# Kernel optimization log

Measured on AMD Instinct MI355X. Metric: run time of the kernel, lower is better.

The kernel has to match this reference:

```python
import jax, jax.numpy as jnp
import numpy as np
import itertools

B, N, K, G = 1024, 1024, 6, 720  # G = K!
H1, H2, C = 64, 32, 40
IN = K * 3


def setup_inputs() -> dict:
    key = jax.random.key(0)
    ks = jax.random.split(key, 8)
    x = jax.random.normal(ks[0], (B, N, 3), dtype=jnp.float32)
    # per-sample subsample indices (torch uses randperm(N)[:K]; distinctness
    # is irrelevant to the math, randint keeps them in-range)
    idx = jax.random.randint(ks[1], (B, K), 0, N)
    perms = jnp.asarray(
        np.array(list(itertools.permutations(range(K))), dtype=np.int32)
    )  # (G, K)
    # MLP params: torch Linear default init ~ U(-1/sqrt(fan_in), 1/sqrt(fan_in))
    def lin(k, fin, fout):
        kw, kb = jax.random.split(k)
        s = 1.0 / np.sqrt(fin)
        W = jax.random.uniform(kw, (fin, fout), jnp.float32, -s, s)
        b = jax.random.uniform(kb, (fout,), jnp.float32, -s, s)
        return W, b
    W1, b1 = lin(ks[2], IN, H1)
    W2, b2 = lin(ks[3], H1, H2)
    W3, b3 = lin(ks[4], H2, C)
    return dict(x=x, W1=W1, b1=b1, W2=W2, b2=b2, W3=W3, b3=b3,
                idx=idx, perms=perms)


def reference(x, W1, b1, W2, b2, W3, b3, idx, perms):
    Bv = x.shape[0]
    Gv, Kv = perms.shape
    # gather the K subsampled points per batch element: (B, K, 3)
    pts = jnp.take_along_axis(x, idx[:, :, None], axis=1)
    # expand over all K! permutations of the point ordering: (B, G, K, 3)
    permuted = pts[:, perms, :]
    flat = permuted.reshape(Bv, Gv, Kv * 3)  # (B, G, K*3)
    h = jax.nn.relu(flat @ W1 + b1)          # (B, G, H1)
    h = jax.nn.relu(h @ W2 + b2)             # (B, G, H2)
    y = h @ W3 + b3                          # (B, G, C)
    return y.mean(axis=1)                    # (B, C)
```

## Files before the change

kernel.cpp:

```cpp
#include <hip/hip_runtime.h>
#include <hip/hip_bf16.h>

typedef __attribute__((ext_vector_type(8))) short short8;
typedef __attribute__((ext_vector_type(4))) float f32x4;
typedef unsigned int u32;
typedef __attribute__((ext_vector_type(4))) unsigned int u32x4;

#define NN 1024

#define LFENCE { asm volatile("s_waitcnt lgkmcnt(0)" ::: "memory"); __builtin_amdgcn_sched_barrier(0); }

#define PKROW(DST, TA, TB) { \
  float va_ = fmaxf(bx_ + (TA), 0.0f), vb_ = fmaxf(bx_ + (TB), 0.0f); \
  asm("v_cvt_pk_bf16_f32 %0, %1, %2" : "=v"(DST) : "v"(va_), "v"(vb_)); }

#define PK3(KA,KB,KC, BX) { const float bx_ = (BX); \
  PKROW(KA, T0_, T1_) PKROW(KB, T2_, T3_) PKROW(KC, T4_, T5_) }

#define SGCOMP(A0,A1,A2, M0,M1,M2) { \
  const float f0_ = b1v + P[(A0)*6+0]; \
  const float f1_ = b1v + P[(A1)*6+0]; \
  const float f2_ = b1v + P[(A2)*6+0]; \
  const float g12_ = P[(A1)*6+1] + P[(A2)*6+2]; \
  const float g21_ = P[(A2)*6+1] + P[(A1)*6+2]; \
  const float g02_ = P[(A0)*6+1] + P[(A2)*6+2]; \
  const float g20_ = P[(A2)*6+1] + P[(A0)*6+2]; \
  const float g01_ = P[(A0)*6+1] + P[(A1)*6+2]; \
  const float g10_ = P[(A1)*6+1] + P[(A0)*6+2]; \
  const float e0_ = P[(M0)*6+3], e1_ = P[(M1)*6+3], e2_ = P[(M2)*6+3]; \
  const float h12_ = P[(M1)*6+4] + P[(M2)*6+5]; \
  const float h21_ = P[(M2)*6+4] + P[(M1)*6+5]; \
  const float h02_ = P[(M0)*6+4] + P[(M2)*6+5]; \
  const float h20_ = P[(M2)*6+4] + P[(M0)*6+5]; \
  const float h01_ = P[(M0)*6+4] + P[(M1)*6+5]; \
  const float h10_ = P[(M1)*6+4] + P[(M0)*6+5]; \
  const float T0_ = e0_+h12_, T1_ = e0_+h21_, T2_ = e1_+h02_; \
  const float T3_ = e1_+h20_, T4_ = e2_+h01_, T5_ = e2_+h10_; \
  PK3(k0,k1,k2,   f0_+g12_)  PK3(k3,k4,k5,   f0_+g21_) \
  PK3(k6,k7,k8,   f1_+g02_)  PK3(k9,k10,k11, f1_+g20_) \
  PK3(k12,k13,k14,f2_+g01_)  PK3(k15,k16,k17,f2_+g10_) }

#define WRT16(BB) { \
  bp0[(BB+0)*64]=k0;  bp0[(BB+8)*64]=k8;  \
  bp1[(BB+1)*64]=k1;  bp1[(BB+9)*64]=k9;  \
  bp2[(BB+2)*64]=k2;  bp2[(BB+10)*64]=k10; \
  bp3[(BB+3)*64]=k3;  bp3[(BB+11)*64]=k11; \
  bp4[(BB+4)*64]=k4;  bp4[(BB+12)*64]=k12; \
  bp5[(BB+5)*64]=k5;  bp5[(BB+13)*64]=k13; \
  bp6[(BB+6)*64]=k6;  bp6[(BB+14)*64]=k14; \
  bp7[(BB+7)*64]=k7;  bp7[(BB+15)*64]=k15; }

#define WOV(RA, RB) { \
  wb[(RA)*64 + (lane ^ ((((RA)) & 7) << 3))] = k16; \
  wb[(RB)*64 + (lane ^ ((((RB)) & 7) << 3))] = k17; }

#define MFMA4T(A0_, A1_) do { \
  f32x4 c0_ = {b2v0,b2v0,b2v0,b2v0}; \
  f32x4 c1_ = {b2v1,b2v1,b2v1,b2v1}; \
  c0_ = __builtin_amdgcn_mfma_f32_16x16x32_bf16(A0_, bh00, c0_, 0,0,0); \
  c0_ = __builtin_amdgcn_mfma_f32_16x16x32_bf16(A1_, bh10, c0_, 0,0,0); \
  c1_ = __builtin_amdgcn_mfma_f32_16x16x32_bf16(A0_, bh01, c1_, 0,0,0); \
  c1_ = __builtin_amdgcn_mfma_f32_16x16x32_bf16(A1_, bh11, c1_, 0,0,0); \
  acc0[0]+=fmaxf(c0_[0],0.f); acc0[1]+=fmaxf(c0_[1],0.f); \
  acc0[2]+=fmaxf(c0_[2],0.f); acc0[3]+=fmaxf(c0_[3],0.f); \
  acc1[0]+=fmaxf(c1_[0],0.f); acc1[1]+=fmaxf(c1_[1],0.f); \
  acc1[2]+=fmaxf(c1_[2],0.f); acc1[3]+=fmaxf(c1_[3],0.f); \
} while(0)

#define RQ(B) { \
  q0  = *(const u32x4*)&wb[(B)+e0b];       q1  = *(const u32x4*)&wb[(B)+e0b+4]; \
  q2  = *(const u32x4*)&wb[(B)+e1b];       q3  = *(const u32x4*)&wb[(B)+e1b+4]; \
  q4  = *(const u32x4*)&wb[(B)+512+e0b];   q5  = *(const u32x4*)&wb[(B)+512+e0b+4]; \
  q6  = *(const u32x4*)&wb[(B)+512+e1b];   q7  = *(const u32x4*)&wb[(B)+512+e1b+4]; \
  q8  = *(const u32x4*)&wb[(B)+1024+e0b];  q9  = *(const u32x4*)&wb[(B)+1024+e0b+4]; \
  q10 = *(const u32x4*)&wb[(B)+1024+e1b];  q11 = *(const u32x4*)&wb[(B)+1024+e1b+4]; }

#define FRAG(dst, qa_, qb_) { \
  u32x4 t_; \
  t_[0] = __builtin_amdgcn_perm(qa_[1], qa_[0], sel); \
  t_[1] = __builtin_amdgcn_perm(qa_[3], qa_[2], sel); \
  t_[2] = __builtin_amdgcn_perm(qb_[1], qb_[0], sel); \
  t_[3] = __builtin_amdgcn_perm(qb_[3], qb_[2], sel); \
  dst = __builtin_bit_cast(short8, t_); }

#define M3 { \
  short8 A0f_, A1f_; \
  FRAG(A0f_, q0, q1);   FRAG(A1f_, q2, q3);   MFMA4T(A0f_, A1f_); \
  FRAG(A0f_, q4, q5);   FRAG(A1f_, q6, q7);   MFMA4T(A0f_, A1f_); \
  FRAG(A0f_, q8, q9);   FRAG(A1f_, q10, q11); MFMA4T(A0f_, A1f_); }

#define ZPAD6 { \
  wb[18*64+(lane^16)]=0u; wb[19*64+(lane^24)]=0u; wb[20*64+(lane^32)]=0u; \
  wb[21*64+(lane^40)]=0u; wb[22*64+(lane^48)]=0u; wb[23*64+(lane^56)]=0u; }

#define MKB(dst_h, KH, NIDX) do { \
  _Pragma("unroll") \
  for (int e_ = 0; e_ < 8; ++e_) { \
    float f_ = W2[((KH)*32 + kg*8 + e_)*32 + 16*(NIDX) + colb]; \
    __hip_bfloat16 hi_ = __float2bfloat16(f_); \
    dst_h[e_] = *(short*)&hi_; \
  } \
} while(0)

__global__ __launch_bounds__(256, 2) void symm_mlp_kernel(
    const float* __restrict__ x,
    const float* __restrict__ W1, const float* __restrict__ b1,
    const float* __restrict__ W2, const float* __restrict__ b2,
    const float* __restrict__ W3, const float* __restrict__ b3,
    const int* __restrict__ idx,
    float* __restrict__ out)
{
    __shared__ u32 h1s[4][72 * 64];
    __shared__ float redbuf[4][32];

    const int tid   = threadIdx.x;
    const int lane  = tid & 63;
    const int wv    = tid >> 6;
    const int batch = blockIdx.x;

    int pidx[6];
    #pragma unroll
    for (int k = 0; k < 6; ++k) pidx[k] = idx[batch * 6 + k];

    float px[6][3];
    #pragma unroll
    for (int k = 0; k < 6; ++k)
        #pragma unroll
        for (int d = 0; d < 3; ++d) px[k][d] = x[(batch * NN + pidx[k]) * 3 + d];

    float w1c[18];
    #pragma unroll
    for (int r = 0; r < 18; ++r) w1c[r] = W1[r * 64 + lane];

    const float b1v = b1[lane];
    const int colb = lane & 15, kg = lane >> 4;
    const float b2v0 = b2[colb];
    const float b2v1 = b2[16 + colb];

    short8 bh00, bh10, bh01, bh11;
    MKB(bh00, 0, 0);
    MKB(bh10, 1, 0);
    MKB(bh01, 0, 1);
    MKB(bh11, 1, 1);

    float P[36];
    #pragma unroll
    for (int k = 0; k < 6; ++k)
    #pragma unroll
    for (int j = 0; j < 6; ++j)
        P[k*6+j] = fmaf(px[k][2], w1c[3*j+2], fmaf(px[k][1], w1c[3*j+1], px[k][0] * w1c[3*j+0]));

    u32* wb  = &h1s[wv][0];
    u32* bp0 = wb + (lane ^ 0);
    u32* bp1 = wb + (lane ^ 8);
    u32* bp2 = wb + (lane ^ 16);
    u32* bp3 = wb + (lane ^ 24);
    u32* bp4 = wb + (lane ^ 32);
    u32* bp5 = wb + (lane ^ 40);
    u32* bp6 = wb + (lane ^ 48);
    u32* bp7 = wb + (lane ^ 56);

    const int r2l = (lane & 15) >> 1;
    const int sm  = r2l << 3;
    const int e0b = r2l * 64 + ((kg * 8) ^ sm);
    const int e1b = r2l * 64 + ((32 + kg * 8) ^ sm);
    const u32 sel = (lane & 1) ? 0x07060302u : 0x05040100u;

    f32x4 acc0 = {0.f,0.f,0.f,0.f}, acc1 = {0.f,0.f,0.f,0.f};
    u32x4 q0,q1,q2,q3,q4,q5,q6,q7,q8,q9,q10,q11;
    u32 k0,k1,k2,k3,k4,k5,k6,k7,k8,k9,k10,k11,k12,k13,k14,k15,k16,k17;

    if (wv == 0) {
        SGCOMP(0,1,2, 3,4,5); WRT16(0);  WOV(64,65);
        SGCOMP(0,1,3, 2,4,5); WRT16(16); WOV(66,67);
        SGCOMP(0,1,4, 2,3,5); WRT16(32); WOV(68,69);
        SGCOMP(0,1,5, 2,3,4); WRT16(48); WOV(70,71);
    } else if (wv == 1) {
        SGCOMP(0,2,4, 1,3,5); WRT16(0);  WOV(64,65);
        SGCOMP(0,2,5, 1,3,4); WRT16(16); WOV(66,67);
        SGCOMP(0,3,4, 1,2,5); WRT16(32); WOV(68,69);
        SGCOMP(0,3,5, 1,2,4); WRT16(48); WOV(70,71);
    } else if (wv == 2) {
        SGCOMP(1,2,3, 0,4,5); WRT16(0);  WOV(64,65);
        SGCOMP(1,2,4, 0,3,5); WRT16(16); WOV(66,67);
        SGCOMP(1,2,5, 0,3,4); WRT16(32); WOV(68,69);
        SGCOMP(1,3,4, 0,2,5); WRT16(48); WOV(70,71);
    } else {
        SGCOMP(1,4,5, 0,2,3); WRT16(0);  WOV(64,65);
        SGCOMP(2,3,4, 0,1,5); WRT16(16); WOV(66,67);
        SGCOMP(2,3,5, 0,1,4); WRT16(32); WOV(68,69);
        SGCOMP(2,4,5, 0,1,3); WRT16(48); WOV(70,71);
    }
    RQ(0);    LFENCE; M3;
    RQ(1536);         M3;
    RQ(3072);         M3;

    ZPAD6;
    if (wv == 0)      { SGCOMP(0,2,3, 1,4,5); }
    else if (wv == 1) { SGCOMP(0,4,5, 1,2,3); }
    else if (wv == 2) { SGCOMP(1,3,5, 0,2,4); }
    else              { SGCOMP(3,4,5, 0,1,2); }
    WRT16(0); WOV(16,17);
    RQ(0); LFENCE; M3;

    float s0 = acc0[0] + acc0[1] + acc0[2] + acc0[3];
    float s1 = acc1[0] + acc1[1] + acc1[2] + acc1[3];
    s0 += __shfl_xor(s0, 16, 64);  s0 += __shfl_xor(s0, 32, 64);
    s1 += __shfl_xor(s1, 16, 64);  s1 += __shfl_xor(s1, 32, 64);
    s0 -= 12.0f * fmaxf(b2v0, 0.0f);
    s1 -= 12.0f * fmaxf(b2v1, 0.0f);

    if (lane < 16)       redbuf[wv][lane] = s0;
    else if (lane < 32)  redbuf[wv][lane] = s1;
    __syncthreads();

    if (tid < 40) {
        float m[32];
        #pragma unroll
        for (int c = 0; c < 32; ++c)
            m[c] = (redbuf[0][c] + redbuf[1][c] + redbuf[2][c] + redbuf[3][c]) * (1.0f / 720.0f);
        float y = b3[tid];
        #pragma unroll
        for (int c = 0; c < 32; ++c) y = fmaf(m[c], W3[c * 40 + tid], y);
        out[batch * 40 + tid] = y;
    }
}

extern "C" void kernel_launch(void* const* d_in, const int* in_sizes, int n_in,
                              void* d_out, int out_size, void* d_ws, size_t ws_size,
                              hipStream_t stream) {
    const float* x  = (const float*)d_in[0];
    const float* W1 = (const float*)d_in[1];
    const float* b1 = (const float*)d_in[2];
    const float* W2 = (const float*)d_in[3];
    const float* b2 = (const float*)d_in[4];
    const float* W3 = (const float*)d_in[5];
    const float* b3 = (const float*)d_in[6];
    const int* idx   = (const int*)d_in[7];
    float* out = (float*)d_out;

    symm_mlp_kernel<<<1024, 256, 0, stream>>>(x, W1, b1, W2, b2, W3, b3, idx, out);
}
```

Baseline: 18.98 us.

## Process permutation chunks one at a time in a small LDS buffer

Each wave now builds, stores and consumes one 18-row chunk of first-layer activations at a time, using a 24-row LDS buffer, instead of staging four chunks in a 72-row buffer. The padding rows are zeroed once up front, and the bias-padding correction grows to 60 rows to match. Cutting LDS per block and raising launch bounds to 3 blocks per SM is meant to increase occupancy. In exchange, the per-chunk LDS store, fence and read sequence is serialized five times, so less write/read work can overlap within a wave.

After: 21.68 us. 1.14x slower.

```diff
diff --git a/kernel.cpp b/kernel.cpp
--- a/kernel.cpp
+++ b/kernel.cpp
@@ -40,19 +40,19 @@
   PK3(k6,k7,k8,   f1_+g02_)  PK3(k9,k10,k11, f1_+g20_) \
   PK3(k12,k13,k14,f2_+g01_)  PK3(k15,k16,k17,f2_+g10_) }
 
-#define WRT16(BB) { \
-  bp0[(BB+0)*64]=k0;  bp0[(BB+8)*64]=k8;  \
-  bp1[(BB+1)*64]=k1;  bp1[(BB+9)*64]=k9;  \
-  bp2[(BB+2)*64]=k2;  bp2[(BB+10)*64]=k10; \
-  bp3[(BB+3)*64]=k3;  bp3[(BB+11)*64]=k11; \
-  bp4[(BB+4)*64]=k4;  bp4[(BB+12)*64]=k12; \
-  bp5[(BB+5)*64]=k5;  bp5[(BB+13)*64]=k13; \
-  bp6[(BB+6)*64]=k6;  bp6[(BB+14)*64]=k14; \
-  bp7[(BB+7)*64]=k7;  bp7[(BB+15)*64]=k15; }
-
-#define WOV(RA, RB) { \
-  wb[(RA)*64 + (lane ^ ((((RA)) & 7) << 3))] = k16; \
-  wb[(RB)*64 + (lane ^ ((((RB)) & 7) << 3))] = k17; }
+#define WRT16 { \
+  bp0[0*64]=k0;  bp0[8*64]=k8;  \
+  bp1[1*64]=k1;  bp1[9*64]=k9;  \
+  bp2[2*64]=k2;  bp2[10*64]=k10; \
+  bp3[3*64]=k3;  bp3[11*64]=k11; \
+  bp4[4*64]=k4;  bp4[12*64]=k12; \
+  bp5[5*64]=k5;  bp5[13*64]=k13; \
+  bp6[6*64]=k6;  bp6[14*64]=k14; \
+  bp7[7*64]=k7;  bp7[15*64]=k15; }
+
+#define WOV { \
+  wb[16*64 + (lane ^ 0)] = k16; \
+  wb[17*64 + (lane ^ 8)] = k17; }
 
 #define MFMA4T(A0_, A1_) do { \
   f32x4 c0_ = {b2v0,b2v0,b2v0,b2v0}; \
@@ -67,13 +67,13 @@
   acc1[2]+=fmaxf(c1_[2],0.f); acc1[3]+=fmaxf(c1_[3],0.f); \
 } while(0)
 
-#define RQ(B) { \
-  q0  = *(const u32x4*)&wb[(B)+e0b];       q1  = *(const u32x4*)&wb[(B)+e0b+4]; \
-  q2  = *(const u32x4*)&wb[(B)+e1b];       q3  = *(const u32x4*)&wb[(B)+e1b+4]; \
-  q4  = *(const u32x4*)&wb[(B)+512+e0b];   q5  = *(const u32x4*)&wb[(B)+512+e0b+4]; \
-  q6  = *(const u32x4*)&wb[(B)+512+e1b];   q7  = *(const u32x4*)&wb[(B)+512+e1b+4]; \
-  q8  = *(const u32x4*)&wb[(B)+1024+e0b];  q9  = *(const u32x4*)&wb[(B)+1024+e0b+4]; \
-  q10 = *(const u32x4*)&wb[(B)+1024+e1b];  q11 = *(const u32x4*)&wb[(B)+1024+e1b+4]; }
+#define RQ { \
+  q0  = *(const u32x4*)&wb[e0b];         q1  = *(const u32x4*)&wb[e0b+4]; \
+  q2  = *(const u32x4*)&wb[e1b];         q3  = *(const u32x4*)&wb[e1b+4]; \
+  q4  = *(const u32x4*)&wb[512+e0b];     q5  = *(const u32x4*)&wb[512+e0b+4]; \
+  q6  = *(const u32x4*)&wb[512+e1b];     q7  = *(const u32x4*)&wb[512+e1b+4]; \
+  q8  = *(const u32x4*)&wb[1024+e0b];    q9  = *(const u32x4*)&wb[1024+e0b+4]; \
+  q10 = *(const u32x4*)&wb[1024+e1b];    q11 = *(const u32x4*)&wb[1024+e1b+4]; }
 
 #define FRAG(dst, qa_, qb_) { \
   u32x4 t_; \
@@ -89,9 +89,8 @@
   FRAG(A0f_, q4, q5);   FRAG(A1f_, q6, q7);   MFMA4T(A0f_, A1f_); \
   FRAG(A0f_, q8, q9);   FRAG(A1f_, q10, q11); MFMA4T(A0f_, A1f_); }
 
-#define ZPAD6 { \
-  wb[18*64+(lane^16)]=0u; wb[19*64+(lane^24)]=0u; wb[20*64+(lane^32)]=0u; \
-  wb[21*64+(lane^40)]=0u; wb[22*64+(lane^48)]=0u; wb[23*64+(lane^56)]=0u; }
+#define CHUNK1(A0,A1,A2, M0,M1,M2) { \
+  SGCOMP(A0,A1,A2, M0,M1,M2); WRT16; WOV; RQ; LFENCE; M3; }
 
 #define MKB(dst_h, KH, NIDX) do { \
   _Pragma("unroll") \
@@ -102,7 +101,7 @@
   } \
 } while(0)
 
-__global__ __launch_bounds__(256, 2) void symm_mlp_kernel(
+__global__ __launch_bounds__(256, 3) void symm_mlp_kernel(
     const float* __restrict__ x,
     const float* __restrict__ W1, const float* __restrict__ b1,
     const float* __restrict__ W2, const float* __restrict__ b2,
@@ -110,7 +109,7 @@
     const int* __restrict__ idx,
     float* __restrict__ out)
 {
-    __shared__ u32 h1s[4][72 * 64];
+    __shared__ u32 h1s[4][24 * 64];
     __shared__ float redbuf[4][32];
 
     const int tid   = threadIdx.x;
@@ -118,24 +117,33 @@
     const int wv    = tid >> 6;
     const int batch = blockIdx.x;
 
-    int pidx[6];
-    #pragma unroll
-    for (int k = 0; k < 6; ++k) pidx[k] = idx[batch * 6 + k];
-
-    float px[6][3];
-    #pragma unroll
-    for (int k = 0; k < 6; ++k)
-        #pragma unroll
-        for (int d = 0; d < 3; ++d) px[k][d] = x[(batch * NN + pidx[k]) * 3 + d];
-
-    float w1c[18];
-    #pragma unroll
-    for (int r = 0; r < 18; ++r) w1c[r] = W1[r * 64 + lane];
-
     const float b1v = b1[lane];
     const int colb = lane & 15, kg = lane >> 4;
     const float b2v0 = b2[colb];
     const float b2v1 = b2[16 + colb];
+
+    float P[36];
+    {
+        int pidx[6];
+        #pragma unroll
+        for (int k = 0; k < 6; ++k) pidx[k] = idx[batch * 6 + k];
+
+        float px[6][3];
+        #pragma unroll
+        for (int k = 0; k < 6; ++k)
+            #pragma unroll
+            for (int d = 0; d < 3; ++d) px[k][d] = x[(batch * NN + pidx[k]) * 3 + d];
+
+        float w1c[18];
+        #pragma unroll
+        for (int r = 0; r < 18; ++r) w1c[r] = W1[r * 64 + lane];
+
+        #pragma unroll
+        for (int k = 0; k < 6; ++k)
+        #pragma unroll
+        for (int j = 0; j < 6; ++j)
+            P[k*6+j] = fmaf(px[k][2], w1c[3*j+2], fmaf(px[k][1], w1c[3*j+1], px[k][0] * w1c[3*j+0]));
+    }
 
     short8 bh00, bh10, bh01, bh11;
     MKB(bh00, 0, 0);
@@ -143,14 +151,10 @@
     MKB(bh01, 0, 1);
     MKB(bh11, 1, 1);
 
-    float P[36];
-    #pragma unroll
-    for (int k = 0; k < 6; ++k)
-    #pragma unroll
-    for (int j = 0; j < 6; ++j)
-        P[k*6+j] = fmaf(px[k][2], w1c[3*j+2], fmaf(px[k][1], w1c[3*j+1], px[k][0] * w1c[3*j+0]));
-
-    u32* wb  = &h1s[wv][0];
+    u32* wb = &h1s[wv][0];
+    wb[18*64+(lane^16)]=0u; wb[19*64+(lane^24)]=0u; wb[20*64+(lane^32)]=0u;
+    wb[21*64+(lane^40)]=0u; wb[22*64+(lane^48)]=0u; wb[23*64+(lane^56)]=0u;
+
     u32* bp0 = wb + (lane ^ 0);
     u32* bp1 = wb + (lane ^ 8);
     u32* bp2 = wb + (lane ^ 16);
@@ -171,44 +175,25 @@
     u32 k0,k1,k2,k3,k4,k5,k6,k7,k8,k9,k10,k11,k12,k13,k14,k15,k16,k17;
 
     if (wv == 0) {
-        SGCOMP(0,1,2, 3,4,5); WRT16(0);  WOV(64,65);
-        SGCOMP(0,1,3, 2,4,5); WRT16(16); WOV(66,67);
-        SGCOMP(0,1,4, 2,3,5); WRT16(32); WOV(68,69);
-        SGCOMP(0,1,5, 2,3,4); WRT16(48); WOV(70,71);
+        CHUNK1(0,1,2, 3,4,5); CHUNK1(0,1,3, 2,4,5); CHUNK1(0,1,4, 2,3,5);
+        CHUNK1(0,1,5, 2,3,4); CHUNK1(0,2,3, 1,4,5);
     } else if (wv == 1) {
-        SGCOMP(0,2,4, 1,3,5); WRT16(0);  WOV(64,65);
-        SGCOMP(0,2,5, 1,3,4); WRT16(16); WOV(66,67);
-        SGCOMP(0,3,4, 1,2,5); WRT16(32); WOV(68,69);
-        SGCOMP(0,3,5, 1,2,4); WRT16(48); WOV(70,71);
+        CHUNK1(0,2,4, 1,3,5); CHUNK1(0,2,5, 1,3,4); CHUNK1(0,3,4, 1,2,5);
+        CHUNK1(0,3,5, 1,2,4); CHUNK1(0,4,5, 1,2,3);
     } else if (wv == 2) {
-        SGCOMP(1,2,3, 0,4,5); WRT16(0);  WOV(64,65);
-        SGCOMP(1,2,4, 0,3,5); WRT16(16); WOV(66,67);
-        SGCOMP(1,2,5, 0,3,4); WRT16(32); WOV(68,69);
-        SGCOMP(1,3,4, 0,2,5); WRT16(48); WOV(70,71);
+        CHUNK1(1,2,3, 0,4,5); CHUNK1(1,2,4, 0,3,5); CHUNK1(1,2,5, 0,3,4);
+        CHUNK1(1,3,4, 0,2,5); CHUNK1(1,3,5, 0,2,4);
     } else {
-        SGCOMP(1,4,5, 0,2,3); WRT16(0);  WOV(64,65);
-        SGCOMP(2,3,4, 0,1,5); WRT16(16); WOV(66,67);
-        SGCOMP(2,3,5, 0,1,4); WRT16(32); WOV(68,69);
-        SGCOMP(2,4,5, 0,1,3); WRT16(48); WOV(70,71);
+        CHUNK1(1,4,5, 0,2,3); CHUNK1(2,3,4, 0,1,5); CHUNK1(2,3,5, 0,1,4);
+        CHUNK1(2,4,5, 0,1,3); CHUNK1(3,4,5, 0,1,2);
     }
-    RQ(0);    LFENCE; M3;
-    RQ(1536);         M3;
-    RQ(3072);         M3;
-
-    ZPAD6;
-    if (wv == 0)      { SGCOMP(0,2,3, 1,4,5); }
-    else if (wv == 1) { SGCOMP(0,4,5, 1,2,3); }
-    else if (wv == 2) { SGCOMP(1,3,5, 0,2,4); }
-    else              { SGCOMP(3,4,5, 0,1,2); }
-    WRT16(0); WOV(16,17);
-    RQ(0); LFENCE; M3;
 
     float s0 = acc0[0] + acc0[1] + acc0[2] + acc0[3];
     float s1 = acc1[0] + acc1[1] + acc1[2] + acc1[3];
     s0 += __shfl_xor(s0, 16, 64);  s0 += __shfl_xor(s0, 32, 64);
     s1 += __shfl_xor(s1, 16, 64);  s1 += __shfl_xor(s1, 32, 64);
-    s0 -= 12.0f * fmaxf(b2v0, 0.0f);
-    s1 -= 12.0f * fmaxf(b2v1, 0.0f);
+    s0 -= 60.0f * fmaxf(b2v0, 0.0f);
+    s1 -= 60.0f * fmaxf(b2v1, 0.0f);
 
     if (lane < 16)       redbuf[wv][lane] = s0;
     else if (lane < 32)  redbuf[wv][lane] = s1;
```
